# Kernel tuning notes

Hardware: AMD Instinct MI355X
Metric: run time of the kernel (lower is better)

Reference implementation:

```python
import jax, jax.numpy as jnp
import numpy as np

B, S, HID, H, D = 2, 2048, 2048, 16, 128
ROPE_THETA = 10000.0
NEG = -1e9


def _rope_tables(seq_len, dim, theta):
    inv_freq = 1.0 / (theta ** (jnp.arange(0, dim, 2, dtype=jnp.float32) / dim))
    t = jnp.arange(seq_len, dtype=jnp.float32)
    freqs = jnp.outer(t, inv_freq)                 # [S, D/2]
    emb = jnp.concatenate([freqs, freqs], axis=-1)  # [S, D]
    return jnp.cos(emb), jnp.sin(emb)


def _rotate_half(x):
    x1, x2 = jnp.split(x, 2, axis=-1)
    return jnp.concatenate([-x2, x1], axis=-1)


def setup_inputs() -> dict:
    key = jax.random.key(0)
    ks = jax.random.split(key, 12)
    hidden_states = jax.random.normal(ks[0], (B, S, HID), dtype=jnp.float32)
    Wq = jax.random.normal(ks[1], (HID, HID), dtype=jnp.float32) * 0.02
    Wk = jax.random.normal(ks[2], (HID, HID), dtype=jnp.float32) * 0.02
    Wv = jax.random.normal(ks[3], (HID, HID), dtype=jnp.float32) * 0.02
    Wo = jax.random.normal(ks[4], (HID, HID), dtype=jnp.float32) * 0.02
    bq = jnp.zeros((HID,), jnp.float32)
    bk = jnp.zeros((HID,), jnp.float32)
    bv = jnp.zeros((HID,), jnp.float32)
    beta = jax.random.normal(ks[5], (1,), dtype=jnp.float32)
    M = jax.random.normal(ks[6], (H, D, D), dtype=jnp.float32) * 0.01
    z = jax.random.uniform(ks[7], (H, D), dtype=jnp.float32) + 1.0  # strictly positive normalizer
    causal = jnp.tril(jnp.ones((S, S), dtype=bool))
    attention_mask = jnp.broadcast_to(
        jnp.where(causal, 0.0, NEG).astype(jnp.float32)[None, None], (B, 1, S, S)
    ) + jnp.zeros((B, 1, S, S), jnp.float32)
    position_ids = jnp.broadcast_to(jnp.arange(S, dtype=jnp.int32), (B, S))
    return {
        "hidden_states": hidden_states, "Wq": Wq, "bq": bq, "Wk": Wk, "bk": bk,
        "Wv": Wv, "bv": bv, "Wo": Wo, "beta": beta, "M": M, "z": z,
        "attention_mask": attention_mask, "position_ids": position_ids,
    }


def reference(hidden_states, Wq, bq, Wk, bk, Wv, bv, Wo, beta, M, z,
              attention_mask, position_ids):
    bsz, seq, hid = hidden_states.shape
    h, d = M.shape[0], M.shape[1]

    # projections (weights stored [in, out])
    q = (hidden_states @ Wq + bq).reshape(bsz, seq, h, d).transpose(0, 2, 1, 3)  # [b,h,s,d]
    k = (hidden_states @ Wk + bk).reshape(bsz, seq, h, d).transpose(0, 2, 1, 3)
    v = (hidden_states @ Wv + bv).reshape(bsz, seq, h, d).transpose(0, 2, 1, 3)

    # RoPE
    cos, sin = _rope_tables(seq, d, ROPE_THETA)          # [s, d]
    cos = cos[position_ids][:, None]                      # [b,1,s,d]
    sin = sin[position_ids][:, None]
    q = q * cos + _rotate_half(q) * sin
    k = k * cos + _rotate_half(k) * sin

    sigma = lambda x: jax.nn.elu(x) + 1.0
    sig_q = sigma(q)
    sig_k = sigma(k)

    # compressive-memory retrieval (uses pre-update M, z)
    mem_num = jnp.einsum('bhsd,hde->bhse', sig_q, M)
    mem_den = jnp.einsum('bhsd,hd->bhs', sig_q, z)
    memory_output = mem_num / mem_den[..., None]

    # memory update via outer products of feature-mapped keys and values
    M_new = M + jnp.einsum('bhsd,bhse->hde', sig_k, v)
    z_new = z + sig_k.sum(axis=(0, 2))

    # local causal attention
    scores = jnp.einsum('bhqd,bhkd->bhqk', q, k) / jnp.sqrt(jnp.float32(d))
    scores = scores + attention_mask
    attn = jax.nn.softmax(scores, axis=-1)
    attn_output = jnp.einsum('bhqk,bhkd->bhqd', attn, v)

    # gated long-term injection
    g = jax.nn.sigmoid(beta)[0]
    combined = g * memory_output + (1.0 - g) * attn_output

    combined = combined.transpose(0, 2, 1, 3).reshape(bsz, seq, h * d)
    final_output = combined @ Wo
    return (final_output, M_new, z_new)
```

## Files before the change

### kernel.cpp

```cpp
#include <hip/hip_runtime.h>


typedef float  floatx4 __attribute__((ext_vector_type(4)));
typedef __bf16 bf16x8  __attribute__((ext_vector_type(8)));

#define DEV __device__ __forceinline__

constexpr int BN  = 2;
constexpr int SS  = 2048;
constexpr int HID = 2048;
constexpr int NH  = 16;
constexpr int DD  = 128;
constexpr int BS  = BN * SS;

DEV unsigned short f2bf(float f) {
  unsigned int u = __float_as_uint(f);
  u += 0x7FFFu + ((u >> 16) & 1u);
  return (unsigned short)(u >> 16);
}
DEV float bf2f(unsigned short h) {
  return __uint_as_float(((unsigned int)h) << 16);
}
DEV float sigma_f(float x) { return x > 0.f ? x + 1.f : __expf(x); }

DEV void cp16(const unsigned short* g, unsigned short* l) {
  __builtin_amdgcn_global_load_lds(
      (const __attribute__((address_space(1))) unsigned int*)g,
      (__attribute__((address_space(3))) unsigned int*)l, 16, 0, 0);
}

DEV bf16x8 scale8(bf16x8 x, float s) {
  bf16x8 r;
  #pragma unroll
  for (int i = 0; i < 8; i++) r[i] = (__bf16)((float)x[i] * s);
  return r;
}

DEV floatx4 mfma16(bf16x8 a, bf16x8 b, floatx4 c) {
  return __builtin_amdgcn_mfma_f32_16x16x32_bf16(a, b, c, 0, 0, 0);
}

constexpr size_t WS_WOT   = 0;
constexpr size_t WS_HSB   = WS_WOT   + (size_t)HID * HID * 2;
constexpr size_t WS_WQT   = WS_HSB   + (size_t)BS  * HID * 2;
constexpr size_t WS_WKT   = WS_WQT   + (size_t)HID * HID * 2;
constexpr size_t WS_WVT   = WS_WKT   + (size_t)HID * HID * 2;
constexpr size_t WS_QB    = WS_WVT   + (size_t)HID * HID * 2;
constexpr size_t WS_KB    = WS_QB    + (size_t)BS  * HID * 2;
constexpr size_t WS_VB    = WS_KB    + (size_t)BS  * HID * 2;
constexpr size_t WS_VTB   = WS_VB    + (size_t)BS  * HID * 2;
constexpr size_t WS_ATT   = WS_VTB   + (size_t)BS  * HID * 2;
constexpr size_t WS_COMB  = WS_ATT   + (size_t)BS  * HID * 2;
constexpr size_t WS_MPART = WS_COMB  + (size_t)BS  * HID * 2;
constexpr size_t WS_ZPART = WS_MPART + (size_t)16 * NH * DD * DD * 4;
constexpr size_t WS_MTB   = WS_ZPART + (size_t)16 * NH * DD * 4;

__global__ __launch_bounds__(256) void k_prep(const float* __restrict__ hs,
                                              const float* __restrict__ Wq, const float* __restrict__ Wk,
                                              const float* __restrict__ Wv, const float* __restrict__ Wo,
                                              const float* __restrict__ M,
                                              unsigned short* __restrict__ hsb,
                                              unsigned short* tq, unsigned short* tk,
                                              unsigned short* tv, unsigned short* to_,
                                              unsigned short* __restrict__ mtb) {
  __shared__ float tile[64][65];
  const int tid = threadIdx.x;
  if (blockIdx.z == 5) {
    if (blockIdx.y >= 16 || blockIdx.x >= 4) return;
    int h = blockIdx.y;
    int d0 = (blockIdx.x & 1) * 64, e0 = (blockIdx.x >> 1) * 64;
    const float* Mh = M + (size_t)h * DD * DD;
    #pragma unroll
    for (int i = 0; i < 16; i++) {
      int idx = i * 256 + tid; int r = idx >> 6, c = idx & 63;
      tile[r][c] = Mh[(size_t)(d0 + r) * DD + e0 + c];
    }
    __syncthreads();
    #pragma unroll
    for (int i = 0; i < 16; i++) {
      int idx = i * 256 + tid; int r = idx >> 6, c = idx & 63;
      mtb[((size_t)h * DD + e0 + r) * DD + d0 + c] = f2bf(tile[c][r]);
    }
    return;
  }
  if (blockIdx.z == 4) {
    int cid = blockIdx.y * 32 + blockIdx.x;
    const float4* src = (const float4*)hs;
    ushort4* dst = (ushort4*)hsb;
    #pragma unroll
    for (int i = 0; i < 8; i++) {
      int idx = cid * 2048 + i * 256 + tid;
      float4 v = src[idx];
      ushort4 o; o.x = f2bf(v.x); o.y = f2bf(v.y); o.z = f2bf(v.z); o.w = f2bf(v.w);
      dst[idx] = o;
    }
    return;
  }
  const float* W; unsigned short* T;
  switch (blockIdx.z) {
    case 0:  W = Wq; T = tq; break;
    case 1:  W = Wk; T = tk; break;
    case 2:  W = Wv; T = tv; break;
    default: W = Wo; T = to_; break;
  }
  int k0 = blockIdx.y * 64, n0 = blockIdx.x * 64;
  #pragma unroll
  for (int i = 0; i < 16; i++) {
    int idx = i * 256 + tid; int r = idx >> 6, c = idx & 63;
    tile[r][c] = W[(size_t)(k0 + r) * HID + n0 + c];
  }
  __syncthreads();
  #pragma unroll
  for (int i = 0; i < 16; i++) {
    int idx = i * 256 + tid; int r = idx >> 6, c = idx & 63;
    T[(size_t)(n0 + r) * HID + k0 + c] = f2bf(tile[c][r]);
  }
}

constexpr int GBM = 256, GBN = 128, GBK = 32;
constexpr int NTK = HID / GBK;
constexpr int A_U    = GBM * GBK;
constexpr int SLOT_U = (GBM + GBN) * GBK;

DEV void stage_slot(const unsigned short* __restrict__ X,
                    const unsigned short* __restrict__ Wt,
                    unsigned short* slot, int m0, int n0, int k0, int tid) {
  #pragma unroll
  for (int i = 0; i < 2; i++) {
    int c = i * 512 + tid;
    int q = c >> 3, p = c & 7, t = p ^ (q & 7);
    int row = 2 * q + (t >> 2), col = k0 + ((t & 3) << 3);
    cp16(X + (size_t)(m0 + row) * HID + col, slot + c * 8);
  }
  {
    int c = tid;
    int q = c >> 3, p = c & 7, t = p ^ (q & 7);
    int row = 2 * q + (t >> 2), col = k0 + ((t & 3) << 3);
    cp16(Wt + (size_t)(n0 + row) * HID + col, slot + A_U + c * 8);
  }
}

DEV bf16x8 ldfrag(const unsigned short* base, int r, int grp) {
  int q = r >> 1;
  int p = (((r & 1) << 2) | grp) ^ (q & 7);
  return __builtin_bit_cast(bf16x8, *(const uint4*)(base + q * 64 + p * 8));
}

DEV void gemm_core(const unsigned short* __restrict__ X,
                   const unsigned short* __restrict__ Wt,
                   unsigned short* lds, int m0, int n0, floatx4 acc[4][4]) {
  const int tid = threadIdx.x;
  const int lane = tid & 63, w = tid >> 6;
  const int grp = lane >> 4, l16 = lane & 15;
  const int wm = (w >> 1) * 64, wn = (w & 1) * 64;
  #pragma unroll
  for (int i = 0; i < 4; i++)
    #pragma unroll
    for (int j = 0; j < 4; j++) acc[i][j] = floatx4{0.f, 0.f, 0.f, 0.f};
  stage_slot(X, Wt, lds,          m0, n0, 0,   tid);
  stage_slot(X, Wt, lds + SLOT_U, m0, n0, GBK, tid);
  int sl_r = 0, sl_w = 2;
  for (int t = 0; t < NTK; t++) {
    if (t + 1 < NTK) asm volatile("s_waitcnt vmcnt(3)" ::: "memory");
    else             asm volatile("s_waitcnt vmcnt(0)" ::: "memory");
    __builtin_amdgcn_s_barrier();
    asm volatile("" ::: "memory");
    if (t + 2 < NTK)
      stage_slot(X, Wt, lds + sl_w * SLOT_U, m0, n0, (t + 2) * GBK, tid);
    const unsigned short* As = lds + sl_r * SLOT_U;
    const unsigned short* Bs = As + A_U;
    bf16x8 af[4], bfr[4];
    #pragma unroll
    for (int mi = 0; mi < 4; mi++) af[mi]  = ldfrag(As, wm + mi * 16 + l16, grp);
    #pragma unroll
    for (int ni = 0; ni < 4; ni++) bfr[ni] = ldfrag(Bs, wn + ni * 16 + l16, grp);
    __builtin_amdgcn_s_setprio(1);
    #pragma unroll
    for (int mi = 0; mi < 4; mi++)
      #pragma unroll
      for (int ni = 0; ni < 4; ni++)
        acc[mi][ni] = mfma16(af[mi], bfr[ni], acc[mi][ni]);
    __builtin_amdgcn_s_setprio(0);
    asm volatile("" ::: "memory");
    sl_r = (sl_r == 2) ? 0 : sl_r + 1;
    sl_w = (sl_w == 2) ? 0 : sl_w + 1;
  }
}

__global__ __launch_bounds__(512, 4) void k_gemm_qkv(
    const unsigned short* __restrict__ Xb,
    const unsigned short* __restrict__ Wtq, const unsigned short* __restrict__ Wtk,
    const unsigned short* __restrict__ Wtv,
    const float* __restrict__ bq, const float* __restrict__ bk, const float* __restrict__ bv,
    unsigned short* __restrict__ qb, unsigned short* __restrict__ kb,
    unsigned short* __restrict__ vb, unsigned short* __restrict__ vtb) {
  const unsigned short* Wt; const float* bias; unsigned short* out;
  switch (blockIdx.z) {
    case 0:  Wt = Wtq; bias = bq; out = qb; break;
    case 1:  Wt = Wtk; bias = bk; out = kb; break;
    default: Wt = Wtv; bias = bv; out = vb; break;
  }
  __shared__ __align__(16) unsigned short lds[3 * SLOT_U];
  int lin = blockIdx.y * 16 + blockIdx.x;
  lin = (lin & 7) * 32 + (lin >> 3);
  int m0 = (lin >> 4) * GBM, n0 = (lin & 15) * GBN;
  floatx4 acc[4][4];
  gemm_core(Xb, Wt, lds, m0, n0, acc);
  const int lane = threadIdx.x & 63, w = threadIdx.x >> 6;
  const int grp = lane >> 4, l16 = lane & 15;
  const int wm = (w >> 1) * 64, wn = (w & 1) * 64;
  const bool isv = (blockIdx.z == 2);
  #pragma unroll
  for (int mi = 0; mi < 4; mi++) {
    int gr0 = m0 + wm + mi * 16;
    int bi  = gr0 >> 11;
    int ssb = (gr0 & 2047) + grp * 4;
    #pragma unroll
    for (int ni = 0; ni < 4; ni++) {
      int col = n0 + wn + ni * 16 + l16;
      float bb_ = bias[col];
      int hh = col >> 7, dd = col & 127;
      ushort4 pk;
      unsigned short* pv = (unsigned short*)&pk;
      #pragma unroll
      for (int r = 0; r < 4; r++) {
        unsigned short val = f2bf(acc[mi][ni][r] + bb_);
        out[(((size_t)(bi * NH + hh)) * SS + ssb + r) * DD + dd] = val;
        pv[r] = val;
      }
      if (isv)
        *(ushort4*)(vtb + (((size_t)(bi * NH + hh)) * DD + dd) * SS + ssb) = pk;
    }
  }
}

__global__ __launch_bounds__(512, 4) void k_gemm_out(const unsigned short* __restrict__ Xb,
                                                     const unsigned short* __restrict__ Wt,
                                                     float* __restrict__ outf) {
  __shared__ __align__(16) unsigned short lds[3 * SLOT_U];
  int lin = blockIdx.y * 16 + blockIdx.x;
  lin = (lin & 7) * 32 + (lin >> 3);
  int m0 = (lin >> 4) * GBM, n0 = (lin & 15) * GBN;
  floatx4 acc[4][4];
  gemm_core(Xb, Wt, lds, m0, n0, acc);
  const int lane = threadIdx.x & 63, w = threadIdx.x >> 6;
  const int grp = lane >> 4, l16 = lane & 15;
  const int wm = (w >> 1) * 64, wn = (w & 1) * 64;
  #pragma unroll
  for (int mi = 0; mi < 4; mi++)
    #pragma unroll
    for (int ni = 0; ni < 4; ni++) {
      int col = n0 + wn + ni * 16 + l16;
      #pragma unroll
      for (int r = 0; r < 4; r++) {
        int gr = m0 + wm + mi * 16 + grp * 4 + r;
        outf[(size_t)gr * HID + col] = acc[mi][ni][r];
      }
    }
}

__global__ __launch_bounds__(256) void k_rope(unsigned short* __restrict__ qb,
                                              unsigned short* __restrict__ kb) {
  int row = blockIdx.x * 4 + (threadIdx.x >> 6);
  int d = threadIdx.x & 63;
  int s = row & (SS - 1);
  size_t base = (size_t)row * DD;
  float ang = (float)s * __expf(-(float)d * (9.210340371976184f / 64.f));
  float sn, c;
  __sincosf(ang, &sn, &c);
  float q1 = bf2f(qb[base + d]), q2 = bf2f(qb[base + d + 64]);
  qb[base + d]      = f2bf(q1 * c - q2 * sn);
  qb[base + d + 64] = f2bf(q2 * c + q1 * sn);
  float k1 = bf2f(kb[base + d]), k2 = bf2f(kb[base + d + 64]);
  kb[base + d]      = f2bf(k1 * c - k2 * sn);
  kb[base + d + 64] = f2bf(k2 * c + k1 * sn);
}

DEV void stage_kv(const unsigned short* __restrict__ Kg,
                  const unsigned short* __restrict__ Vg,
                  unsigned short* Klb, unsigned short* Vtlb, int tid) {
  #pragma unroll
  for (int i = 0; i < 4; i++) {
    int c = i * 256 + tid;
    int kv = c >> 4, ck = c & 15;
    cp16(Kg + kv * DD + ((ck ^ (kv & 7)) << 3), Klb + c * 8);
    int dvt = c >> 3, cv = c & 7;
    cp16(Vg + (size_t)dvt * SS + ((cv ^ (dvt & 7)) << 3), Vtlb + c * 8);
  }
}

DEV void attn_update(const unsigned short* Kl, const unsigned short* Vtl,
                     unsigned short* Plw, const bf16x8* qf, floatx4* o,
                     floatx4* lacc, bool diag, int grp, int l16, int wrow) {
  const int swk = l16 & 7;
  floatx4 sacc[4];
  #pragma unroll
  for (int j = 0; j < 4; j++) sacc[j] = floatx4{0.f, 0.f, 0.f, 0.f};
  __builtin_amdgcn_s_setprio(1);
  #pragma unroll
  for (int ks = 0; ks < 4; ks++)
    #pragma unroll
    for (int j = 0; j < 4; j++) {
      bf16x8 kf = __builtin_bit_cast(bf16x8,
          *(const uint4*)(Kl + (j * 16 + l16) * 128 + (((ks * 4 + grp) ^ swk) << 3)));
      sacc[j] = __builtin_amdgcn_mfma_f32_16x16x32_bf16(qf[ks], kf, sacc[j], 0, 0, 0);
    }
  __builtin_amdgcn_s_setprio(0);
  #pragma unroll
  for (int j = 0; j < 4; j++)
    #pragma unroll
    for (int r = 0; r < 4; r++) {
      float p = (diag && (j * 16 + l16) > (wrow + grp * 4 + r)) ? 0.f : __expf(sacc[j][r]);
      Plw[(j >> 1) * 640 + (grp * 4 + r) * 40 + (j & 1) * 16 + l16] = f2bf(p);
    }
  const bf16x8 ones = __builtin_bit_cast(bf16x8,
      uint4{0x3F803F80u, 0x3F803F80u, 0x3F803F80u, 0x3F803F80u});
  __builtin_amdgcn_s_setprio(1);
  #pragma unroll
  for (int ks2 = 0; ks2 < 2; ks2++) {
    bf16x8 pf = __builtin_bit_cast(bf16x8,
        *(const uint4*)(Plw + ks2 * 640 + l16 * 40 + grp * 8));
    *lacc = __builtin_amdgcn_mfma_f32_16x16x32_bf16(pf, ones, *lacc, 0, 0, 0);
    #pragma unroll
    for (int n = 0; n < 8; n++) {
      bf16x8 vf = __builtin_bit_cast(bf16x8,
          *(const uint4*)(Vtl + (n * 16 + l16) * 64 + (((ks2 * 4 + grp) ^ swk) << 3)));
      o[n] = __builtin_amdgcn_mfma_f32_16x16x32_bf16(pf, vf, o[n], 0, 0, 0);
    }
  }
  __builtin_amdgcn_s_setprio(0);
}

__global__ __launch_bounds__(256) void k_attn(const unsigned short* __restrict__ qb,
                                              const unsigned short* __restrict__ kb,
                                              const unsigned short* __restrict__ vtb,
                                              unsigned short* __restrict__ attb) {
  const int t = blockIdx.x, bh = blockIdx.y;
  const int qtA = t, qtB = 31 - t;
  const int tid = threadIdx.x, w = tid >> 6, lane = tid & 63;
  const int grp = lane >> 4, l16 = lane & 15;
  const unsigned short* Q  = qb  + (size_t)bh * SS * DD;
  const unsigned short* K  = kb  + (size_t)bh * SS * DD;
  const unsigned short* VT = vtb + (size_t)bh * DD * SS;
  __shared__ __align__(16) unsigned short Kl[2][64 * 128];
  __shared__ __align__(16) unsigned short Vtl[2][128 * 64];
  __shared__ __align__(16) unsigned short Pl[4][1280];
  const float sc = 0.08838834764831845f;
  bf16x8 qfA[4], qfB[4];
  {
    int qrA = qtA * 64 + w * 16 + l16, qrB = qtB * 64 + w * 16 + l16;
    #pragma unroll
    for (int ks = 0; ks < 4; ks++) {
      qfA[ks] = scale8(__builtin_bit_cast(bf16x8, *(const uint4*)(Q + (size_t)qrA * DD + ks * 32 + grp * 8)), sc);
      qfB[ks] = scale8(__builtin_bit_cast(bf16x8, *(const uint4*)(Q + (size_t)qrB * DD + ks * 32 + grp * 8)), sc);
    }
  }
  floatx4 oA[8], oB[8];
  #pragma unroll
  for (int n = 0; n < 8; n++) { oA[n] = floatx4{0,0,0,0}; oB[n] = floatx4{0,0,0,0}; }
  floatx4 laccA = floatx4{0,0,0,0}, laccB = floatx4{0,0,0,0};
  stage_kv(K, VT, Kl[0], Vtl[0], tid);
  asm volatile("s_waitcnt vmcnt(0)" ::: "memory");
  __builtin_amdgcn_s_barrier();
  int cur = 0;
  for (int kt = 0; kt <= qtB; kt++) {
    asm volatile("" ::: "memory");
    if (kt < qtB)
      stage_kv(K + (size_t)(kt + 1) * 64 * DD, VT + (size_t)(kt + 1) * 64,
               Kl[cur ^ 1], Vtl[cur ^ 1], tid);
    attn_update(Kl[cur], Vtl[cur], Pl[w], qfB, oB, &laccB, kt == qtB, grp, l16, w * 16);
    if (kt <= qtA)
      attn_update(Kl[cur], Vtl[cur], Pl[w], qfA, oA, &laccA, kt == qtA, grp, l16, w * 16);
    asm volatile("" ::: "memory");
    if (kt < qtB) {
      asm volatile("s_waitcnt vmcnt(0)" ::: "memory");
      __builtin_amdgcn_s_barrier();
    }
    cur ^= 1;
  }
  #pragma unroll
  for (int r = 0; r < 4; r++) {
    float invA = 1.f / laccA[r], invB = 1.f / laccB[r];
    int rA = qtA * 64 + w * 16 + grp * 4 + r;
    int rB = qtB * 64 + w * 16 + grp * 4 + r;
    #pragma unroll
    for (int n = 0; n < 8; n++) {
      attb[(size_t)bh * SS * DD + (size_t)rA * DD + n * 16 + l16] = f2bf(oA[n][r] * invA);
      attb[(size_t)bh * SS * DD + (size_t)rB * DD + n * 16 + l16] = f2bf(oB[n][r] * invB);
    }
  }
}

__global__ __launch_bounds__(256) void k_memcomb(const unsigned short* __restrict__ qb,
                                                 const unsigned short* __restrict__ mtb,
                                                 const float* __restrict__ z,
                                                 const float* __restrict__ beta,
                                                 const unsigned short* __restrict__ attb,
                                                 unsigned short* __restrict__ comb) {
  const int st = blockIdx.x, bh = blockIdx.y;
  const int b = bh >> 4, h = bh & 15;
  const int tid = threadIdx.x, w = tid >> 6, lane = tid & 63;
  const int grp = lane >> 4, l16 = lane & 15;
  const int s0 = st * 64;
  __shared__ __align__(16) unsigned short qtl[64 * 128];
  __shared__ __align__(16) unsigned short sqt[64 * 128];
  __shared__ float zf[128];
  __shared__ float den[64];
  #pragma unroll
  for (int i = 0; i < 4; i++) {
    int c = i * 256 + tid;
    int row = c >> 4, ch = c & 15;
    cp16(qb + ((size_t)bh * SS + s0 + row) * DD + ch * 8, qtl + c * 8);
  }
  if (tid < 32) {
    #pragma unroll
    for (int j = 0; j < 4; j++) zf[tid * 4 + j] = z[h * DD + tid * 4 + j];
  }
  asm volatile("s_waitcnt vmcnt(0)" ::: "memory");
  __syncthreads();
  #pragma unroll
  for (int i = 0; i < 4; i++) {
    int c = i * 256 + tid;
    int row = c >> 4, ch = c & 15;
    bf16x8 v = __builtin_bit_cast(bf16x8, *(const uint4*)(qtl + c * 8));
    unsigned short o8[8];
    float dp = 0.f;
    #pragma unroll
    for (int j = 0; j < 8; j++) {
      float sgv = sigma_f((float)v[j]);
      dp += sgv * zf[ch * 8 + j];
      o8[j] = f2bf(sgv);
    }
    *(uint4*)(sqt + ((size_t)row * 128 + (size_t)(ch ^ (row & 15)) * 8)) =
        *(const uint4*)o8;
    #pragma unroll
    for (int msk = 1; msk < 16; msk <<= 1) dp += __shfl_xor(dp, msk, 64);
    if (l16 == 0) den[row] = dp;
  }
  __syncthreads();
  floatx4 acc[4][2];
  #pragma unroll
  for (int mi = 0; mi < 4; mi++)
    #pragma unroll
    for (int ni = 0; ni < 2; ni++) acc[mi][ni] = floatx4{0.f, 0.f, 0.f, 0.f};
  const unsigned short* Mh = mtb + (size_t)h * DD * DD;
  #pragma unroll
  for (int k = 0; k < 4; k++) {
    bf16x8 af[4], bfr[2];
    #pragma unroll
    for (int mi = 0; mi < 4; mi++)
      af[mi] = __builtin_bit_cast(bf16x8,
          *(const uint4*)(sqt + (size_t)(mi * 16 + l16) * 128 + (size_t)((k * 4 + grp) ^ l16) * 8));
    #pragma unroll
    for (int ni = 0; ni < 2; ni++)
      bfr[ni] = __builtin_bit_cast(bf16x8,
          *(const uint4*)(Mh + (size_t)(w * 32 + ni * 16 + l16) * DD + k * 32 + grp * 8));
    #pragma unroll
    for (int mi = 0; mi < 4; mi++)
      #pragma unroll
      for (int ni = 0; ni < 2; ni++)
        acc[mi][ni] = mfma16(af[mi], bfr[ni], acc[mi][ni]);
  }
  float g = 1.f / (1.f + __expf(-beta[0]));
  #pragma unroll
  for (int mi = 0; mi < 4; mi++)
    #pragma unroll
    for (int ni = 0; ni < 2; ni++) {
      int col = w * 32 + ni * 16 + l16;
      #pragma unroll
      for (int r = 0; r < 4; r++) {
        int srow = mi * 16 + grp * 4 + r;
        float mo = acc[mi][ni][r] / den[srow];
        float at = bf2f(attb[((size_t)bh * SS + s0 + srow) * DD + col]);
        comb[((size_t)(b * SS + s0 + srow)) * HID + h * DD + col] = f2bf(g * mo + (1.f - g) * at);
      }
    }
}

__global__ __launch_bounds__(256) void k_mnew(const unsigned short* __restrict__ kb,
                                              const unsigned short* __restrict__ vb,
                                              float* __restrict__ mpart,
                                              float* __restrict__ zpart) {
  const int ch = blockIdx.x, h = blockIdx.y;
  const int tid = threadIdx.x;
  const int td = tid >> 4, te = tid & 15;
  __shared__ float sk[16][128], vv[16][128];
  float acc[8][8];
  float zacc = 0.f;
  #pragma unroll
  for (int a = 0; a < 8; a++)
    #pragma unroll
    for (int b2 = 0; b2 < 8; b2++) acc[a][b2] = 0.f;
  for (int c0 = 0; c0 < 256; c0 += 16) {
    __syncthreads();
    #pragma unroll
    for (int i = 0; i < 8; i++) {
      int idx = i * 256 + tid; int r = idx >> 7, cc = idx & 127;
      int bs = ch * 256 + c0 + r;
      size_t addr = ((size_t)((bs >> 11) * NH + h) * SS + (bs & 2047)) * DD + cc;
      float skv = sigma_f(bf2f(kb[addr]));
      sk[r][cc] = skv;
      zacc += skv;
      vv[r][cc] = bf2f(vb[addr]);
    }
    __syncthreads();
    for (int i = 0; i < 16; i++) {
      float ks_[8], vs_[8];
      #pragma unroll
      for (int a = 0; a < 8; a++) ks_[a] = sk[i][td * 8 + a];
      #pragma unroll
      for (int b2 = 0; b2 < 8; b2++) vs_[b2] = vv[i][te * 8 + b2];
      #pragma unroll
      for (int a = 0; a < 8; a++)
        #pragma unroll
        for (int b2 = 0; b2 < 8; b2++) acc[a][b2] += ks_[a] * vs_[b2];
    }
  }
  float* mp = mpart + ((size_t)ch * NH + h) * DD * DD;
  #pragma unroll
  for (int a = 0; a < 8; a++)
    #pragma unroll
    for (int b2 = 0; b2 < 8; b2++)
      mp[(size_t)(td * 8 + a) * DD + te * 8 + b2] = acc[a][b2];
  __syncthreads();
  float* red = (float*)sk;
  red[tid] = zacc;
  __syncthreads();
  if (tid < 128)
    zpart[((size_t)ch * NH + h) * DD + tid] = red[tid] + red[tid + 128];
}

__global__ __launch_bounds__(256) void k_mreduce(const float* __restrict__ M,
                                                 const float* __restrict__ mpart,
                                                 const float* __restrict__ z,
                                                 const float* __restrict__ zpart,
                                                 float* __restrict__ outM,
                                                 float* __restrict__ outz) {
  int idx = blockIdx.x * 256 + threadIdx.x;
  float s = M[idx];
  #pragma unroll
  for (int ch = 0; ch < 16; ch++) s += mpart[(size_t)ch * NH * DD * DD + idx];
  outM[idx] = s;
  if (blockIdx.x < 8) {
    int zi = blockIdx.x * 256 + threadIdx.x;
    float zs = z[zi];
    #pragma unroll
    for (int ch = 0; ch < 16; ch++) zs += zpart[(size_t)ch * NH * DD + zi];
    outz[zi] = zs;
  }
}

extern "C" void kernel_launch(void* const* d_in, const int* in_sizes, int n_in,
                              void* d_out, int out_size, void* d_ws, size_t ws_size,
                              hipStream_t stream) {
  const float* hs   = (const float*)d_in[0];
  const float* Wq   = (const float*)d_in[1];
  const float* bq   = (const float*)d_in[2];
  const float* Wk   = (const float*)d_in[3];
  const float* bk   = (const float*)d_in[4];
  const float* Wv   = (const float*)d_in[5];
  const float* bv   = (const float*)d_in[6];
  const float* Wo   = (const float*)d_in[7];
  const float* beta = (const float*)d_in[8];
  const float* M    = (const float*)d_in[9];
  const float* z    = (const float*)d_in[10];

  char* ws = (char*)d_ws;
  unsigned short* wot  = (unsigned short*)(ws + WS_WOT);
  unsigned short* hsb  = (unsigned short*)(ws + WS_HSB);
  unsigned short* wqt  = (unsigned short*)(ws + WS_WQT);
  unsigned short* wkt  = (unsigned short*)(ws + WS_WKT);
  unsigned short* wvt  = (unsigned short*)(ws + WS_WVT);
  unsigned short* qb   = (unsigned short*)(ws + WS_QB);
  unsigned short* kb   = (unsigned short*)(ws + WS_KB);
  unsigned short* vb   = (unsigned short*)(ws + WS_VB);
  unsigned short* vtb  = (unsigned short*)(ws + WS_VTB);
  unsigned short* attb = (unsigned short*)(ws + WS_ATT);
  unsigned short* comb = (unsigned short*)(ws + WS_COMB);
  float*          mprt = (float*)(ws + WS_MPART);
  float*          zprt = (float*)(ws + WS_ZPART);
  unsigned short* mtb  = (unsigned short*)(ws + WS_MTB);

  float* out_final = (float*)d_out;
  float* out_M = out_final + (size_t)BS * HID;
  float* out_z = out_M + NH * DD * DD;

  k_prep    <<<dim3(32, 32, 6),        256, 0, stream>>>(hs, Wq, Wk, Wv, Wo, M, hsb, wqt, wkt, wvt, wot, mtb);
  k_gemm_qkv<<<dim3(16, 16, 3),        512, 0, stream>>>(hsb, wqt, wkt, wvt, bq, bk, bv, qb, kb, vb, vtb);
  k_rope    <<<dim3(BN * NH * SS / 4), 256, 0, stream>>>(qb, kb);
  k_attn    <<<dim3(16, 32),           256, 0, stream>>>(qb, kb, vtb, attb);
  k_memcomb <<<dim3(32, 32),           256, 0, stream>>>(qb, mtb, z, beta, attb, comb);
  k_gemm_out<<<dim3(16, 16),           512, 0, stream>>>(comb, wot, out_final);
  k_mnew    <<<dim3(16, 16),           256, 0, stream>>>(kb, vb, mprt, zprt);
  k_mreduce <<<dim3(1024),             256, 0, stream>>>(M, mprt, z, zprt, out_M, out_z);
}
```

Measured before the change: 464.3 us.

## Compute memory update with bf16 MFMA using transposed V, drop row-major V store

Rewrites the memory-update kernel so sigma(K)^T·V runs on bf16 MFMA instructions instead of scalar fp32 outer products. It reads V from the already-produced transposed buffer and stages sigma(K) transposed in padded LDS. The z column sums now come from per-thread accumulators reduced with warp shuffles. Because V is now read only in transposed form, the QKV GEMM no longer writes the row-major V copy, which saves global stores. Sigma(K) is rounded to bf16 before the product, which lowers the precision of M_new.

```diff
diff --git a/kernel.cpp b/kernel.cpp
--- a/kernel.cpp
+++ b/kernel.cpp
@@ -193,12 +193,12 @@
     const unsigned short* __restrict__ Wtv,
     const float* __restrict__ bq, const float* __restrict__ bk, const float* __restrict__ bv,
     unsigned short* __restrict__ qb, unsigned short* __restrict__ kb,
-    unsigned short* __restrict__ vb, unsigned short* __restrict__ vtb) {
+    unsigned short* __restrict__ vtb) {
   const unsigned short* Wt; const float* bias; unsigned short* out;
   switch (blockIdx.z) {
     case 0:  Wt = Wtq; bias = bq; out = qb; break;
     case 1:  Wt = Wtk; bias = bk; out = kb; break;
-    default: Wt = Wtv; bias = bv; out = vb; break;
+    default: Wt = Wtv; bias = bv; out = nullptr; break;
   }
   __shared__ __align__(16) unsigned short lds[3 * SLOT_U];
   int lin = blockIdx.y * 16 + blockIdx.x;
@@ -225,7 +225,8 @@
       #pragma unroll
       for (int r = 0; r < 4; r++) {
         unsigned short val = f2bf(acc[mi][ni][r] + bb_);
-        out[(((size_t)(bi * NH + hh)) * SS + ssb + r) * DD + dd] = val;
+        if (!isv)
+          out[(((size_t)(bi * NH + hh)) * SS + ssb + r) * DD + dd] = val;
         pv[r] = val;
       }
       if (isv)
@@ -478,56 +479,83 @@
 }
 
 __global__ __launch_bounds__(256) void k_mnew(const unsigned short* __restrict__ kb,
-                                              const unsigned short* __restrict__ vb,
+                                              const unsigned short* __restrict__ vtb,
                                               float* __restrict__ mpart,
                                               float* __restrict__ zpart) {
   const int ch = blockIdx.x, h = blockIdx.y;
-  const int tid = threadIdx.x;
-  const int td = tid >> 4, te = tid & 15;
-  __shared__ float sk[16][128], vv[16][128];
-  float acc[8][8];
-  float zacc = 0.f;
-  #pragma unroll
-  for (int a = 0; a < 8; a++)
-    #pragma unroll
-    for (int b2 = 0; b2 < 8; b2++) acc[a][b2] = 0.f;
-  for (int c0 = 0; c0 < 256; c0 += 16) {
+  const int tid = threadIdx.x, lane = tid & 63, w = tid >> 6;
+  const int grp = lane >> 4, l16 = lane & 15;
+  const int zs = tid & 31, zdg = tid >> 5;
+  __shared__ __align__(16) unsigned short skT[128 * 40];
+  __shared__ __align__(16) unsigned short vl[128 * 40];
+  const int b = ch >> 3;
+  const int sl0 = (ch & 7) * 256;
+  const unsigned short* Kg = kb  + ((size_t)(b * NH + h) * SS + sl0) * DD;
+  const unsigned short* Vg = vtb + (size_t)(b * NH + h) * DD * SS + sl0;
+  float zacc[16];
+  #pragma unroll
+  for (int j = 0; j < 16; j++) zacc[j] = 0.f;
+  floatx4 acc[2][8];
+  #pragma unroll
+  for (int i = 0; i < 2; i++)
+    #pragma unroll
+    for (int j = 0; j < 8; j++) acc[i][j] = floatx4{0.f, 0.f, 0.f, 0.f};
+  for (int st = 0; st < 8; st++) {
+    const unsigned short* kp = Kg + (size_t)(st * 32 + zs) * DD + zdg * 16;
+    bf16x8 k0 = __builtin_bit_cast(bf16x8, *(const uint4*)kp);
+    bf16x8 k1 = __builtin_bit_cast(bf16x8, *(const uint4*)(kp + 8));
+    int c0 = tid,        e0 = c0 >> 2, q0 = c0 & 3;
+    int c1 = 256 + tid,  e1 = c1 >> 2, q1 = c1 & 3;
+    uint4 vr0 = *(const uint4*)(Vg + (size_t)e0 * SS + st * 32 + q0 * 8);
+    uint4 vr1 = *(const uint4*)(Vg + (size_t)e1 * SS + st * 32 + q1 * 8);
     __syncthreads();
     #pragma unroll
-    for (int i = 0; i < 8; i++) {
-      int idx = i * 256 + tid; int r = idx >> 7, cc = idx & 127;
-      int bs = ch * 256 + c0 + r;
-      size_t addr = ((size_t)((bs >> 11) * NH + h) * SS + (bs & 2047)) * DD + cc;
-      float skv = sigma_f(bf2f(kb[addr]));
-      sk[r][cc] = skv;
-      zacc += skv;
-      vv[r][cc] = bf2f(vb[addr]);
-    }
+    for (int j = 0; j < 8; j++) {
+      float s0 = sigma_f((float)k0[j]);
+      float s1 = sigma_f((float)k1[j]);
+      zacc[j] += s0; zacc[8 + j] += s1;
+      skT[(zdg * 16 + j) * 40 + zs]     = f2bf(s0);
+      skT[(zdg * 16 + 8 + j) * 40 + zs] = f2bf(s1);
+    }
+    *(uint4*)(vl + e0 * 40 + q0 * 8) = vr0;
+    *(uint4*)(vl + e1 * 40 + q1 * 8) = vr1;
     __syncthreads();
-    for (int i = 0; i < 16; i++) {
-      float ks_[8], vs_[8];
+    bf16x8 af[2], bfv[8];
+    #pragma unroll
+    for (int ti = 0; ti < 2; ti++)
+      af[ti] = __builtin_bit_cast(bf16x8,
+          *(const uint4*)(skT + (w * 32 + ti * 16 + l16) * 40 + grp * 8));
+    #pragma unroll
+    for (int tj = 0; tj < 8; tj++)
+      bfv[tj] = __builtin_bit_cast(bf16x8,
+          *(const uint4*)(vl + (tj * 16 + l16) * 40 + grp * 8));
+    __builtin_amdgcn_s_setprio(1);
+    #pragma unroll
+    for (int ti = 0; ti < 2; ti++)
       #pragma unroll
-      for (int a = 0; a < 8; a++) ks_[a] = sk[i][td * 8 + a];
+      for (int tj = 0; tj < 8; tj++)
+        acc[ti][tj] = mfma16(af[ti], bfv[tj], acc[ti][tj]);
+    __builtin_amdgcn_s_setprio(0);
+  }
+  float* mp = mpart + ((size_t)ch * NH + h) * DD * DD;
+  #pragma unroll
+  for (int ti = 0; ti < 2; ti++)
+    #pragma unroll
+    for (int tj = 0; tj < 8; tj++) {
+      int d = w * 32 + ti * 16 + grp * 4;
+      int e = tj * 16 + l16;
       #pragma unroll
-      for (int b2 = 0; b2 < 8; b2++) vs_[b2] = vv[i][te * 8 + b2];
-      #pragma unroll
-      for (int a = 0; a < 8; a++)
-        #pragma unroll
-        for (int b2 = 0; b2 < 8; b2++) acc[a][b2] += ks_[a] * vs_[b2];
-    }
-  }
-  float* mp = mpart + ((size_t)ch * NH + h) * DD * DD;
-  #pragma unroll
-  for (int a = 0; a < 8; a++)
-    #pragma unroll
-    for (int b2 = 0; b2 < 8; b2++)
-      mp[(size_t)(td * 8 + a) * DD + te * 8 + b2] = acc[a][b2];
-  __syncthreads();
-  float* red = (float*)sk;
-  red[tid] = zacc;
-  __syncthreads();
-  if (tid < 128)
-    zpart[((size_t)ch * NH + h) * DD + tid] = red[tid] + red[tid + 128];
+      for (int r = 0; r < 4; r++)
+        mp[(size_t)(d + r) * DD + e] = acc[ti][tj][r];
+    }
+  float* zp = zpart + ((size_t)ch * NH + h) * DD;
+  #pragma unroll
+  for (int j = 0; j < 16; j++) {
+    float v = zacc[j];
+    #pragma unroll
+    for (int msk = 1; msk <= 16; msk <<= 1) v += __shfl_xor(v, msk, 64);
+    if (zs == 0) zp[zdg * 16 + j] = v;
+  }
 }
 
 __global__ __launch_bounds__(256) void k_mreduce(const float* __restrict__ M,
@@ -573,7 +601,6 @@
   unsigned short* wvt  = (unsigned short*)(ws + WS_WVT);
   unsigned short* qb   = (unsigned short*)(ws + WS_QB);
   unsigned short* kb   = (unsigned short*)(ws + WS_KB);
-  unsigned short* vb   = (unsigned short*)(ws + WS_VB);
   unsigned short* vtb  = (unsigned short*)(ws + WS_VTB);
   unsigned short* attb = (unsigned short*)(ws + WS_ATT);
   unsigned short* comb = (unsigned short*)(ws + WS_COMB);
@@ -586,11 +613,11 @@
   float* out_z = out_M + NH * DD * DD;
 
   k_prep    <<<dim3(32, 32, 6),        256, 0, stream>>>(hs, Wq, Wk, Wv, Wo, M, hsb, wqt, wkt, wvt, wot, mtb);
-  k_gemm_qkv<<<dim3(16, 16, 3),        512, 0, stream>>>(hsb, wqt, wkt, wvt, bq, bk, bv, qb, kb, vb, vtb);
+  k_gemm_qkv<<<dim3(16, 16, 3),        512, 0, stream>>>(hsb, wqt, wkt, wvt, bq, bk, bv, qb, kb, vtb);
   k_rope    <<<dim3(BN * NH * SS / 4), 256, 0, stream>>>(qb, kb);
   k_attn    <<<dim3(16, 32),           256, 0, stream>>>(qb, kb, vtb, attb);
   k_memcomb <<<dim3(32, 32),           256, 0, stream>>>(qb, mtb, z, beta, attb, comb);
   k_gemm_out<<<dim3(16, 16),           512, 0, stream>>>(comb, wot, out_final);
-  k_mnew    <<<dim3(16, 16),           256, 0, stream>>>(kb, vb, mprt, zprt);
+  k_mnew    <<<dim3(16, 16),           256, 0, stream>>>(kb, vtb, mprt, zprt);
   k_mreduce <<<dim3(1024),             256, 0, stream>>>(M, mprt, z, zprt, out_M, out_z);
 }
```

After: 431.6 us. -7.0%, faster.
